# Kernel tuning notes

Hardware: AMD Instinct MI355X
Metric: run time of the kernel (lower is better)

The kernel has to match this reference:

```python
import jax, jax.numpy as jnp
import numpy as np

# init_kwargs constants
K = 5                      # kernel_sz
SIGMA_SPATIAL = 2.0
SIGMA_INTENSITY = 0.1
KVAL = -1.0 / (2.0 * SIGMA_SPATIAL ** 2)        # kernel buffer value (same for all k^2 taps)
SIDIV = 1.0 / (2.0 * SIGMA_INTENSITY ** 2)      # sigma_intensity_div


def _extract_block(x, k):
    """F.unfold equivalent: (B,C,H,W) -> (B,H,W,k*k,C), SAME zero padding, row-major taps."""
    B, C, H, W = x.shape
    p = k // 2
    xp = jnp.pad(x, ((0, 0), (0, 0), (p, p), (p, p)))
    # fixed small loop over k*k taps (not a data-dim loop)
    pats = jnp.stack([xp[:, :, i:i + H, j:j + W] for i in range(k) for j in range(k)], axis=2)  # B,C,k2,H,W
    return jnp.transpose(pats, (0, 3, 4, 2, 1))  # B,H,W,k2,C


def setup_inputs() -> dict:
    key = jax.random.key(0)
    k1, k2 = jax.random.split(key)
    template = jax.random.uniform(k1, (1, 3, 1080, 1920), dtype=jnp.float32)
    vector_curr = jax.random.normal(k2, (1, 2, 1080, 1920), dtype=jnp.float32)
    return {"template": template, "vector_curr": vector_curr}


def reference(template, vector_curr):
    # inputs are float32, so cast() is a no-op
    compare_pix = jnp.transpose(template, (0, 2, 3, 1))[:, :, :, None, :]   # B,H,W,1,C
    compare_kernel = _extract_block(template, K)                            # B,H,W,k2,C
    intensity_diff = jnp.sum((compare_pix - compare_kernel) ** 2, axis=-1)  # B,H,W,k2
    coeff = jnp.clip(1.0 - jnp.abs(KVAL - intensity_diff * SIDIV), 0.0, 1.0)[..., None]  # B,H,W,k2,1
    vector_block = _extract_block(vector_curr, K)                           # B,H,W,k2,Cv
    num = jnp.sum(vector_block * coeff, axis=-2)                            # B,H,W,Cv
    den = jnp.sum(coeff, axis=-2)                                           # B,H,W,1
    out = (num / den).astype(jnp.float16)
    return jnp.transpose(out, (0, 3, 1, 2))                                  # B,Cv,H,W fp16
```

## Files before the change

kernel.cpp:

```cpp
#include <hip/hip_runtime.h>


#define IMG_H 1080
#define IMG_W 1920
#define IMG_HW (IMG_H * IMG_W)
#define TS_X 64
#define TS_Y 16
#define HALO_H 20
#define HALO_W 72
#define NCH 5
#define F4_PER_ROW 18
#define F4_PER_CH  (F4_PER_ROW * HALO_H)

typedef float f4u __attribute__((ext_vector_type(4), aligned(4)));

__global__ __launch_bounds__(256)
void jbf_kernel(const float* __restrict__ tpl,
                const float* __restrict__ vec,
                float* __restrict__ out) {
    constexpr float SIDIV = 50.0f;

    __shared__ __align__(16) float smem[NCH][HALO_H][HALO_W];

    const int tid = threadIdx.x;
    const int x0  = blockIdx.x * TS_X;
    const int y0  = blockIdx.y * TS_Y;

    const bool interior = (blockIdx.x >= 1) & (blockIdx.x <= 28) &
                          (blockIdx.y >= 1) & (blockIdx.y <= 66);

    if (interior) {
        const int i0  = tid;
        const int i1  = tid + 256;
        const bool p1 = (i1 < F4_PER_CH);
        const int i1c = p1 ? i1 : 0;
        const int r0 = i0 / F4_PER_ROW, c0 = i0 - r0 * F4_PER_ROW;
        const int r1 = i1c / F4_PER_ROW, c1 = i1c - r1 * F4_PER_ROW;
        const int off0 = r0 * IMG_W + c0 * 4;
        const int off1 = r1 * IMG_W + c1 * 4;
        const int tl   = (y0 - 2) * IMG_W + (x0 - 2);

        f4u v[2 * NCH];
#pragma unroll
        for (int ch = 0; ch < NCH; ++ch) {
            const float* __restrict__ src =
                (ch < 3) ? (tpl + ch * IMG_HW) : (vec + (ch - 3) * IMG_HW);
            v[2 * ch]     = *(const f4u*)(src + tl + off0);
            v[2 * ch + 1] = *(const f4u*)(src + tl + off1);
        }
#pragma unroll
        for (int ch = 0; ch < NCH; ++ch) {
            float4* d0 = (float4*)&smem[ch][r0][c0 * 4];
            d0->x = v[2 * ch].x; d0->y = v[2 * ch].y;
            d0->z = v[2 * ch].z; d0->w = v[2 * ch].w;
            if (p1) {
                float4* d1 = (float4*)&smem[ch][r1][c1 * 4];
                d1->x = v[2 * ch + 1].x; d1->y = v[2 * ch + 1].y;
                d1->z = v[2 * ch + 1].z; d1->w = v[2 * ch + 1].w;
            }
        }
    } else {
#pragma unroll
        for (int c = 0; c < NCH; ++c) {
            const float* __restrict__ src =
                (c < 3) ? (tpl + c * IMG_HW) : (vec + (c - 3) * IMG_HW);
#pragma unroll
            for (int i = tid; i < HALO_H * HALO_W; i += 256) {
                const int r   = i / HALO_W;
                const int col = i - r * HALO_W;
                const int gy  = y0 + r - 2;
                const int gx  = x0 + col - 2;
                float val = 0.0f;
                if (gy >= 0 && gy < IMG_H && gx >= 0 && gx < IMG_W)
                    val = src[gy * IMG_W + gx];
                smem[c][r][col] = val;
            }
        }
    }
    __syncthreads();

    const int tx = tid & 15;
    const int ty = tid >> 4;
    const int lx = tx * 4;

    float num0[4] = {0.f, 0.f, 0.f, 0.f};
    float num1[4] = {0.f, 0.f, 0.f, 0.f};
    float den [4] = {0.f, 0.f, 0.f, 0.f};
    float c0[4], c1[4], c2[4];

#pragma unroll
    for (int s = 0; s < 5; ++s) {
        constexpr int DYS[5] = {2, 0, 1, 3, 4};
        const int row = ty + DYS[s];
        const float4 a0  = *(const float4*)&smem[0][row][lx];
        const float4 b0  = *(const float4*)&smem[0][row][lx + 4];
        const float4 a1  = *(const float4*)&smem[1][row][lx];
        const float4 b1  = *(const float4*)&smem[1][row][lx + 4];
        const float4 a2  = *(const float4*)&smem[2][row][lx];
        const float4 b2  = *(const float4*)&smem[2][row][lx + 4];
        const float4 av0 = *(const float4*)&smem[3][row][lx];
        const float4 bv0 = *(const float4*)&smem[3][row][lx + 4];
        const float4 av1 = *(const float4*)&smem[4][row][lx];
        const float4 bv1 = *(const float4*)&smem[4][row][lx + 4];

        if (s == 0) {
            c0[0] = a0.z; c0[1] = a0.w; c0[2] = b0.x; c0[3] = b0.y;
            c1[0] = a1.z; c1[1] = a1.w; c1[2] = b1.x; c1[3] = b1.y;
            c2[0] = a2.z; c2[1] = a2.w; c2[2] = b2.x; c2[3] = b2.y;
        }

        const float w0[8]  = {a0.x, a0.y, a0.z, a0.w, b0.x, b0.y, b0.z, b0.w};
        const float w1[8]  = {a1.x, a1.y, a1.z, a1.w, b1.x, b1.y, b1.z, b1.w};
        const float w2[8]  = {a2.x, a2.y, a2.z, a2.w, b2.x, b2.y, b2.z, b2.w};
        const float wv0[8] = {av0.x, av0.y, av0.z, av0.w, bv0.x, bv0.y, bv0.z, bv0.w};
        const float wv1[8] = {av1.x, av1.y, av1.z, av1.w, bv1.x, bv1.y, bv1.z, bv1.w};

#pragma unroll
        for (int dx = 0; dx < 5; ++dx) {
#pragma unroll
            for (int px = 0; px < 4; ++px) {
                const int k = dx + px;
                const float d0 = c0[px] - w0[k];
                const float d1 = c1[px] - w1[k];
                const float d2 = c2[px] - w2[k];
                const float id = fmaf(d0, d0, fmaf(d1, d1, d2 * d2));
                const float coeff = fmaxf(fmaf(id, -SIDIV, 0.875f), 0.0f);
                num0[px] = fmaf(wv0[k], coeff, num0[px]);
                num1[px] = fmaf(wv1[k], coeff, num1[px]);
                den [px] += coeff;
            }
        }
    }

    const int gy = y0 + ty;
    if (gy < IMG_H) {
        const int gx = x0 + lx;
        float4 o0, o1;
        const float r0 = __builtin_amdgcn_rcpf(den[0]);
        const float r1 = __builtin_amdgcn_rcpf(den[1]);
        const float r2 = __builtin_amdgcn_rcpf(den[2]);
        const float r3 = __builtin_amdgcn_rcpf(den[3]);
        o0.x = num0[0] * r0; o0.y = num0[1] * r1; o0.z = num0[2] * r2; o0.w = num0[3] * r3;
        o1.x = num1[0] * r0; o1.y = num1[1] * r1; o1.z = num1[2] * r2; o1.w = num1[3] * r3;
        *(float4*)(out + (size_t)0 * IMG_HW + gy * IMG_W + gx) = o0;
        *(float4*)(out + (size_t)1 * IMG_HW + gy * IMG_W + gx) = o1;
    }
}

extern "C" void kernel_launch(void* const* d_in, const int* in_sizes, int n_in,
                              void* d_out, int out_size, void* d_ws, size_t ws_size,
                              hipStream_t stream) {
    const float* tpl = (const float*)d_in[0];
    const float* vec = (const float*)d_in[1];
    float* out = (float*)d_out;

    dim3 grid(IMG_W / TS_X, (IMG_H + TS_Y - 1) / TS_Y);
    jbf_kernel<<<grid, 256, 0, stream>>>(tpl, vec, out);
}
```

Baseline: 111.4 us.

## Process four row tiles per block with double-buffered LDS prefetch

Each block now walks four vertical tiles, prefetching the next tile's halo into registers before computing the current one and writing it into a second shared-memory buffer afterwards. The aim is to hide global load latency behind compute and amortize per-block setup. In exchange the grid shrinks fourfold, shared memory per block doubles, and register pressure rises, which can reduce occupancy and parallelism across CUs.

```diff
diff --git a/kernel.cpp b/kernel.cpp
--- a/kernel.cpp
+++ b/kernel.cpp
@@ -6,13 +6,57 @@
 #define IMG_HW (IMG_H * IMG_W)
 #define TS_X 64
 #define TS_Y 16
+#define NTILE 4
 #define HALO_H 20
 #define HALO_W 72
 #define NCH 5
 #define F4_PER_ROW 18
-#define F4_PER_CH  (F4_PER_ROW * HALO_H)
+#define F4_PER_CH (F4_PER_ROW * HALO_H)
 
 typedef float f4u __attribute__((ext_vector_type(4), aligned(4)));
+
+#define LOAD_TILE(Y0) do {                                                 \
+    const int tl_ = ((Y0) - 2) * IMG_W + (x0 - 2);                         \
+    _Pragma("unroll")                                                      \
+    for (int ch_ = 0; ch_ < NCH; ++ch_) {                                  \
+        const float* __restrict__ src_ =                                   \
+            (ch_ < 3) ? (tpl + ch_ * IMG_HW) : (vec + (ch_ - 3) * IMG_HW); \
+        v[2 * ch_]     = *(const f4u*)(src_ + tl_ + off0);                 \
+        v[2 * ch_ + 1] = *(const f4u*)(src_ + tl_ + off1);                 \
+    }                                                                      \
+} while (0)
+
+#define WRITE_TILE(BUF) do {                                               \
+    _Pragma("unroll")                                                      \
+    for (int ch_ = 0; ch_ < NCH; ++ch_) {                                  \
+        float4* d0_ = (float4*)&smem[(BUF)][ch_][r0][c0 * 4];              \
+        d0_->x = v[2 * ch_].x; d0_->y = v[2 * ch_].y;                      \
+        d0_->z = v[2 * ch_].z; d0_->w = v[2 * ch_].w;                      \
+        if (p1) {                                                          \
+            float4* d1_ = (float4*)&smem[(BUF)][ch_][r1][c1 * 4];          \
+            d1_->x = v[2 * ch_ + 1].x; d1_->y = v[2 * ch_ + 1].y;          \
+            d1_->z = v[2 * ch_ + 1].z; d1_->w = v[2 * ch_ + 1].w;          \
+        }                                                                  \
+    }                                                                      \
+} while (0)
+
+#define BORDER_STAGE(BUF, Y0) do {                                         \
+    _Pragma("unroll")                                                      \
+    for (int ch_ = 0; ch_ < NCH; ++ch_) {                                  \
+        const float* __restrict__ src_ =                                   \
+            (ch_ < 3) ? (tpl + ch_ * IMG_HW) : (vec + (ch_ - 3) * IMG_HW); \
+        for (int i_ = tid; i_ < HALO_H * HALO_W; i_ += 256) {              \
+            const int r_   = i_ / HALO_W;                                  \
+            const int col_ = i_ - r_ * HALO_W;                             \
+            const int gy_  = (Y0) + r_ - 2;                                \
+            const int gx_  = x0 + col_ - 2;                                \
+            float val_ = 0.0f;                                             \
+            if (gy_ >= 0 && gy_ < IMG_H && gx_ >= 0 && gx_ < IMG_W)        \
+                val_ = src_[gy_ * IMG_W + gx_];                            \
+            smem[(BUF)][ch_][r_][col_] = val_;                             \
+        }                                                                  \
+    }                                                                      \
+} while (0)
 
 __global__ __launch_bounds__(256)
 void jbf_kernel(const float* __restrict__ tpl,
@@ -20,130 +64,125 @@
                 float* __restrict__ out) {
     constexpr float SIDIV = 50.0f;
 
-    __shared__ __align__(16) float smem[NCH][HALO_H][HALO_W];
+    __shared__ __align__(16) float smem[2][NCH][HALO_H][HALO_W];
 
     const int tid = threadIdx.x;
-    const int x0  = blockIdx.x * TS_X;
-    const int y0  = blockIdx.y * TS_Y;
+    const int bx  = blockIdx.x;
+    const int x0  = bx * TS_X;
+    const int yb  = blockIdx.y * (TS_Y * NTILE);
+    const bool xin = (bx >= 1) & (bx <= 28);
 
-    const bool interior = (blockIdx.x >= 1) & (blockIdx.x <= 28) &
-                          (blockIdx.y >= 1) & (blockIdx.y <= 66);
-
-    if (interior) {
-        const int i0  = tid;
-        const int i1  = tid + 256;
-        const bool p1 = (i1 < F4_PER_CH);
-        const int i1c = p1 ? i1 : 0;
-        const int r0 = i0 / F4_PER_ROW, c0 = i0 - r0 * F4_PER_ROW;
-        const int r1 = i1c / F4_PER_ROW, c1 = i1c - r1 * F4_PER_ROW;
-        const int off0 = r0 * IMG_W + c0 * 4;
-        const int off1 = r1 * IMG_W + c1 * 4;
-        const int tl   = (y0 - 2) * IMG_W + (x0 - 2);
-
-        f4u v[2 * NCH];
-#pragma unroll
-        for (int ch = 0; ch < NCH; ++ch) {
-            const float* __restrict__ src =
-                (ch < 3) ? (tpl + ch * IMG_HW) : (vec + (ch - 3) * IMG_HW);
-            v[2 * ch]     = *(const f4u*)(src + tl + off0);
-            v[2 * ch + 1] = *(const f4u*)(src + tl + off1);
-        }
-#pragma unroll
-        for (int ch = 0; ch < NCH; ++ch) {
-            float4* d0 = (float4*)&smem[ch][r0][c0 * 4];
-            d0->x = v[2 * ch].x; d0->y = v[2 * ch].y;
-            d0->z = v[2 * ch].z; d0->w = v[2 * ch].w;
-            if (p1) {
-                float4* d1 = (float4*)&smem[ch][r1][c1 * 4];
-                d1->x = v[2 * ch + 1].x; d1->y = v[2 * ch + 1].y;
-                d1->z = v[2 * ch + 1].z; d1->w = v[2 * ch + 1].w;
-            }
-        }
-    } else {
-#pragma unroll
-        for (int c = 0; c < NCH; ++c) {
-            const float* __restrict__ src =
-                (c < 3) ? (tpl + c * IMG_HW) : (vec + (c - 3) * IMG_HW);
-#pragma unroll
-            for (int i = tid; i < HALO_H * HALO_W; i += 256) {
-                const int r   = i / HALO_W;
-                const int col = i - r * HALO_W;
-                const int gy  = y0 + r - 2;
-                const int gx  = x0 + col - 2;
-                float val = 0.0f;
-                if (gy >= 0 && gy < IMG_H && gx >= 0 && gx < IMG_W)
-                    val = src[gy * IMG_W + gx];
-                smem[c][r][col] = val;
-            }
-        }
-    }
-    __syncthreads();
+    const int i1  = tid + 256;
+    const bool p1 = (i1 < F4_PER_CH);
+    const int i1c = p1 ? i1 : 0;
+    const int r0 = tid / F4_PER_ROW, c0 = tid - r0 * F4_PER_ROW;
+    const int r1 = i1c / F4_PER_ROW, c1 = i1c - r1 * F4_PER_ROW;
+    const int off0 = r0 * IMG_W + c0 * 4;
+    const int off1 = r1 * IMG_W + c1 * 4;
 
     const int tx = tid & 15;
     const int ty = tid >> 4;
     const int lx = tx * 4;
 
-    float num0[4] = {0.f, 0.f, 0.f, 0.f};
-    float num1[4] = {0.f, 0.f, 0.f, 0.f};
-    float den [4] = {0.f, 0.f, 0.f, 0.f};
-    float c0[4], c1[4], c2[4];
+    f4u v[10];
 
-#pragma unroll
-    for (int s = 0; s < 5; ++s) {
-        constexpr int DYS[5] = {2, 0, 1, 3, 4};
-        const int row = ty + DYS[s];
-        const float4 a0  = *(const float4*)&smem[0][row][lx];
-        const float4 b0  = *(const float4*)&smem[0][row][lx + 4];
-        const float4 a1  = *(const float4*)&smem[1][row][lx];
-        const float4 b1  = *(const float4*)&smem[1][row][lx + 4];
-        const float4 a2  = *(const float4*)&smem[2][row][lx];
-        const float4 b2  = *(const float4*)&smem[2][row][lx + 4];
-        const float4 av0 = *(const float4*)&smem[3][row][lx];
-        const float4 bv0 = *(const float4*)&smem[3][row][lx + 4];
-        const float4 av1 = *(const float4*)&smem[4][row][lx];
-        const float4 bv1 = *(const float4*)&smem[4][row][lx + 4];
-
-        if (s == 0) {
-            c0[0] = a0.z; c0[1] = a0.w; c0[2] = b0.x; c0[3] = b0.y;
-            c1[0] = a1.z; c1[1] = a1.w; c1[2] = b1.x; c1[3] = b1.y;
-            c2[0] = a2.z; c2[1] = a2.w; c2[2] = b2.x; c2[3] = b2.y;
-        }
-
-        const float w0[8]  = {a0.x, a0.y, a0.z, a0.w, b0.x, b0.y, b0.z, b0.w};
-        const float w1[8]  = {a1.x, a1.y, a1.z, a1.w, b1.x, b1.y, b1.z, b1.w};
-        const float w2[8]  = {a2.x, a2.y, a2.z, a2.w, b2.x, b2.y, b2.z, b2.w};
-        const float wv0[8] = {av0.x, av0.y, av0.z, av0.w, bv0.x, bv0.y, bv0.z, bv0.w};
-        const float wv1[8] = {av1.x, av1.y, av1.z, av1.w, bv1.x, bv1.y, bv1.z, bv1.w};
-
-#pragma unroll
-        for (int dx = 0; dx < 5; ++dx) {
-#pragma unroll
-            for (int px = 0; px < 4; ++px) {
-                const int k = dx + px;
-                const float d0 = c0[px] - w0[k];
-                const float d1 = c1[px] - w1[k];
-                const float d2 = c2[px] - w2[k];
-                const float id = fmaf(d0, d0, fmaf(d1, d1, d2 * d2));
-                const float coeff = fmaxf(fmaf(id, -SIDIV, 0.875f), 0.0f);
-                num0[px] = fmaf(wv0[k], coeff, num0[px]);
-                num1[px] = fmaf(wv1[k], coeff, num1[px]);
-                den [px] += coeff;
-            }
+    {
+        const int y0 = yb;
+        if (xin & (y0 >= 2) & (y0 + 17 < IMG_H)) {
+            LOAD_TILE(y0);
+            WRITE_TILE(0);
+        } else {
+            BORDER_STAGE(0, y0);
         }
     }
 
-    const int gy = y0 + ty;
-    if (gy < IMG_H) {
-        const int gx = x0 + lx;
-        float4 o0, o1;
-        const float r0 = __builtin_amdgcn_rcpf(den[0]);
-        const float r1 = __builtin_amdgcn_rcpf(den[1]);
-        const float r2 = __builtin_amdgcn_rcpf(den[2]);
-        const float r3 = __builtin_amdgcn_rcpf(den[3]);
-        o0.x = num0[0] * r0; o0.y = num0[1] * r1; o0.z = num0[2] * r2; o0.w = num0[3] * r3;
-        o1.x = num1[0] * r0; o1.y = num1[1] * r1; o1.z = num1[2] * r2; o1.w = num1[3] * r3;
-        *(float4*)(out + (size_t)0 * IMG_HW + gy * IMG_W + gx) = o0;
-        *(float4*)(out + (size_t)1 * IMG_HW + gy * IMG_W + gx) = o1;
+    for (int t = 0; t < NTILE; ++t) {
+        const int cur = t & 1;
+        const int y0  = yb + t * TS_Y;
+        const int yn  = y0 + TS_Y;
+        const bool have_next = (t + 1 < NTILE);
+        const bool int_next  = have_next && xin && (yn + 17 < IMG_H);
+
+        if (int_next) LOAD_TILE(yn);
+        __syncthreads();
+
+        {
+            const float (*S)[HALO_H][HALO_W] =
+                (const float (*)[HALO_H][HALO_W])smem[cur];
+
+            float num0[4] = {0.f, 0.f, 0.f, 0.f};
+            float num1[4] = {0.f, 0.f, 0.f, 0.f};
+            float den [4] = {0.f, 0.f, 0.f, 0.f};
+            float cc0[4], cc1[4], cc2[4];
+
+#pragma unroll
+            for (int s = 0; s < 5; ++s) {
+                constexpr int DYS[5] = {2, 0, 1, 3, 4};
+                const int row = ty + DYS[s];
+                const float4 a0  = *(const float4*)&S[0][row][lx];
+                const float4 b0  = *(const float4*)&S[0][row][lx + 4];
+                const float4 a1  = *(const float4*)&S[1][row][lx];
+                const float4 b1  = *(const float4*)&S[1][row][lx + 4];
+                const float4 a2  = *(const float4*)&S[2][row][lx];
+                const float4 b2  = *(const float4*)&S[2][row][lx + 4];
+                const float4 av0 = *(const float4*)&S[3][row][lx];
+                const float4 bv0 = *(const float4*)&S[3][row][lx + 4];
+                const float4 av1 = *(const float4*)&S[4][row][lx];
+                const float4 bv1 = *(const float4*)&S[4][row][lx + 4];
+
+                if (s == 0) {
+                    cc0[0] = a0.z; cc0[1] = a0.w; cc0[2] = b0.x; cc0[3] = b0.y;
+                    cc1[0] = a1.z; cc1[1] = a1.w; cc1[2] = b1.x; cc1[3] = b1.y;
+                    cc2[0] = a2.z; cc2[1] = a2.w; cc2[2] = b2.x; cc2[3] = b2.y;
+                }
+
+                const float w0[8]  = {a0.x, a0.y, a0.z, a0.w, b0.x, b0.y, b0.z, b0.w};
+                const float w1[8]  = {a1.x, a1.y, a1.z, a1.w, b1.x, b1.y, b1.z, b1.w};
+                const float w2[8]  = {a2.x, a2.y, a2.z, a2.w, b2.x, b2.y, b2.z, b2.w};
+                const float wv0[8] = {av0.x, av0.y, av0.z, av0.w, bv0.x, bv0.y, bv0.z, bv0.w};
+                const float wv1[8] = {av1.x, av1.y, av1.z, av1.w, bv1.x, bv1.y, bv1.z, bv1.w};
+
+#pragma unroll
+                for (int dx = 0; dx < 5; ++dx) {
+#pragma unroll
+                    for (int px = 0; px < 4; ++px) {
+                        const int k = dx + px;
+                        const float d0 = cc0[px] - w0[k];
+                        const float d1 = cc1[px] - w1[k];
+                        const float d2 = cc2[px] - w2[k];
+                        const float id = fmaf(d0, d0, fmaf(d1, d1, d2 * d2));
+                        const float coeff = fmaxf(fmaf(id, -SIDIV, 0.875f), 0.0f);
+                        num0[px] = fmaf(wv0[k], coeff, num0[px]);
+                        num1[px] = fmaf(wv1[k], coeff, num1[px]);
+                        den [px] += coeff;
+                    }
+                }
+            }
+
+            const int gy = y0 + ty;
+            if (gy < IMG_H) {
+                const int gx = x0 + lx;
+                float4 o0, o1;
+                const float q0 = __builtin_amdgcn_rcpf(den[0]);
+                const float q1 = __builtin_amdgcn_rcpf(den[1]);
+                const float q2 = __builtin_amdgcn_rcpf(den[2]);
+                const float q3 = __builtin_amdgcn_rcpf(den[3]);
+                o0.x = num0[0] * q0; o0.y = num0[1] * q1;
+                o0.z = num0[2] * q2; o0.w = num0[3] * q3;
+                o1.x = num1[0] * q0; o1.y = num1[1] * q1;
+                o1.z = num1[2] * q2; o1.w = num1[3] * q3;
+                *(float4*)(out + (size_t)0 * IMG_HW + gy * IMG_W + gx) = o0;
+                *(float4*)(out + (size_t)1 * IMG_HW + gy * IMG_W + gx) = o1;
+            }
+        }
+
+        if (have_next) {
+            if (int_next) {
+                WRITE_TILE(1 - cur);
+            } else {
+                BORDER_STAGE(1 - cur, yn);
+            }
+        }
     }
 }
 
@@ -154,6 +193,6 @@
     const float* vec = (const float*)d_in[1];
     float* out = (float*)d_out;
 
-    dim3 grid(IMG_W / TS_X, (IMG_H + TS_Y - 1) / TS_Y);
+    dim3 grid(IMG_W / TS_X, (IMG_H + TS_Y * NTILE - 1) / (TS_Y * NTILE));
     jbf_kernel<<<grid, 256, 0, stream>>>(tpl, vec, out);
 }
```

New measurement: 136.7 us. 1.23x slower.

## Replace shared-memory halo tiling with direct per-thread global loads

Applied to the files above, without the earlier changes.

Removes the LDS staging of the 5-channel halo tile and the __syncthreads barrier. Each thread now loads its 8-wide row windows straight from global memory for each of the 5 stencil rows, relying on L1/L2 caches for reuse between neighbouring threads. Borders are handled with clamped or masked loads. This cuts LDS traffic and the barrier, but issues more global and cache requests per output, and the row loop is left non-unrolled, which can expose load latency.

```diff
diff --git a/kernel.cpp b/kernel.cpp
--- a/kernel.cpp
+++ b/kernel.cpp
@@ -6,13 +6,82 @@
 #define IMG_HW (IMG_H * IMG_W)
 #define TS_X 64
 #define TS_Y 16
-#define HALO_H 20
-#define HALO_W 72
-#define NCH 5
-#define F4_PER_ROW 18
-#define F4_PER_CH  (F4_PER_ROW * HALO_H)
 
 typedef float f4u __attribute__((ext_vector_type(4), aligned(4)));
+
+#define UNPACK8(dst, A, B) \
+    dst[0]=(A).x; dst[1]=(A).y; dst[2]=(A).z; dst[3]=(A).w; \
+    dst[4]=(B).x; dst[5]=(B).y; dst[6]=(B).z; dst[7]=(B).w;
+
+#define LOAD_FAST(ROW) do {                                                   \
+    const float* p_ = tpl + (ROW) * IMG_W + (gx - 2);                         \
+    const float* q_ = vec + (ROW) * IMG_W + (gx - 2);                         \
+    const f4u a0_  = *(const f4u*)(p_);                                       \
+    const f4u b0_  = *(const f4u*)(p_ + 4);                                   \
+    const f4u a1_  = *(const f4u*)(p_ + IMG_HW);                              \
+    const f4u b1_  = *(const f4u*)(p_ + IMG_HW + 4);                          \
+    const f4u a2_  = *(const f4u*)(p_ + 2 * IMG_HW);                          \
+    const f4u b2_  = *(const f4u*)(p_ + 2 * IMG_HW + 4);                      \
+    const f4u av0_ = *(const f4u*)(q_);                                       \
+    const f4u bv0_ = *(const f4u*)(q_ + 4);                                   \
+    const f4u av1_ = *(const f4u*)(q_ + IMG_HW);                              \
+    const f4u bv1_ = *(const f4u*)(q_ + IMG_HW + 4);                          \
+    UNPACK8(w0,  a0_,  b0_)  UNPACK8(w1,  a1_,  b1_)                          \
+    UNPACK8(w2,  a2_,  b2_)  UNPACK8(wv0, av0_, bv0_)                         \
+    UNPACK8(wv1, av1_, bv1_)                                                  \
+} while (0)
+
+#define LOAD_CLAMPY(ROW) do {                                                 \
+    const int   rc_ = (ROW) < 0 ? 0 : ((ROW) > IMG_H - 1 ? IMG_H - 1 : (ROW));\
+    const float m_  = ((ROW) >= 0 && (ROW) < IMG_H) ? 1.0f : 0.0f;            \
+    LOAD_FAST(rc_);                                                           \
+    _Pragma("unroll")                                                         \
+    for (int k_ = 0; k_ < 8; ++k_) {                                          \
+        w0[k_] *= m_; w1[k_] *= m_; w2[k_] *= m_;                             \
+        wv0[k_] *= m_; wv1[k_] *= m_;                                         \
+    }                                                                         \
+} while (0)
+
+#define LOAD_SLOW(ROW) do {                                                   \
+    const bool rv_ = ((ROW) >= 0) & ((ROW) < IMG_H);                          \
+    const int  rb_ = (rv_ ? (ROW) : 0) * IMG_W;                               \
+    _Pragma("unroll")                                                         \
+    for (int k_ = 0; k_ < 8; ++k_) {                                          \
+        const int   col_ = gx - 2 + k_;                                       \
+        const bool  v_   = rv_ & (col_ >= 0) & (col_ < IMG_W);                \
+        const int   ic_  = rb_ + (v_ ? col_ : 0);                             \
+        const float m_   = v_ ? 1.0f : 0.0f;                                  \
+        w0[k_]  = m_ * tpl[ic_];                                              \
+        w1[k_]  = m_ * tpl[ic_ + IMG_HW];                                     \
+        w2[k_]  = m_ * tpl[ic_ + 2 * IMG_HW];                                 \
+        wv0[k_] = m_ * vec[ic_];                                              \
+        wv1[k_] = m_ * vec[ic_ + IMG_HW];                                     \
+    }                                                                         \
+} while (0)
+
+#define LOAD_ROW(ROW) do {                                                    \
+    if (xin & yin)  LOAD_FAST(ROW);                                           \
+    else if (xin)   LOAD_CLAMPY(ROW);                                         \
+    else            LOAD_SLOW(ROW);                                           \
+} while (0)
+
+#define TAPS do {                                                             \
+    _Pragma("unroll")                                                         \
+    for (int dx = 0; dx < 5; ++dx) {                                          \
+        _Pragma("unroll")                                                     \
+        for (int px = 0; px < 4; ++px) {                                      \
+            const int   k  = dx + px;                                         \
+            const float d0 = c0[px] - w0[k];                                  \
+            const float d1 = c1[px] - w1[k];                                  \
+            const float d2 = c2[px] - w2[k];                                  \
+            const float id = fmaf(d0, d0, fmaf(d1, d1, d2 * d2));             \
+            const float coeff = fmaxf(fmaf(id, -SIDIV, 0.875f), 0.0f);        \
+            num0[px] = fmaf(wv0[k], coeff, num0[px]);                         \
+            num1[px] = fmaf(wv1[k], coeff, num1[px]);                         \
+            den [px] += coeff;                                                \
+        }                                                                     \
+    }                                                                         \
+} while (0)
 
 __global__ __launch_bounds__(256)
 void jbf_kernel(const float* __restrict__ tpl,
@@ -20,121 +89,35 @@
                 float* __restrict__ out) {
     constexpr float SIDIV = 50.0f;
 
-    __shared__ __align__(16) float smem[NCH][HALO_H][HALO_W];
+    const int tid = threadIdx.x;
+    const int tx  = tid & 15;
+    const int ty  = tid >> 4;
+    const int gx  = blockIdx.x * TS_X + tx * 4;
+    const int gy  = blockIdx.y * TS_Y + ty;
 
-    const int tid = threadIdx.x;
-    const int x0  = blockIdx.x * TS_X;
-    const int y0  = blockIdx.y * TS_Y;
-
-    const bool interior = (blockIdx.x >= 1) & (blockIdx.x <= 28) &
-                          (blockIdx.y >= 1) & (blockIdx.y <= 66);
-
-    if (interior) {
-        const int i0  = tid;
-        const int i1  = tid + 256;
-        const bool p1 = (i1 < F4_PER_CH);
-        const int i1c = p1 ? i1 : 0;
-        const int r0 = i0 / F4_PER_ROW, c0 = i0 - r0 * F4_PER_ROW;
-        const int r1 = i1c / F4_PER_ROW, c1 = i1c - r1 * F4_PER_ROW;
-        const int off0 = r0 * IMG_W + c0 * 4;
-        const int off1 = r1 * IMG_W + c1 * 4;
-        const int tl   = (y0 - 2) * IMG_W + (x0 - 2);
-
-        f4u v[2 * NCH];
-#pragma unroll
-        for (int ch = 0; ch < NCH; ++ch) {
-            const float* __restrict__ src =
-                (ch < 3) ? (tpl + ch * IMG_HW) : (vec + (ch - 3) * IMG_HW);
-            v[2 * ch]     = *(const f4u*)(src + tl + off0);
-            v[2 * ch + 1] = *(const f4u*)(src + tl + off1);
-        }
-#pragma unroll
-        for (int ch = 0; ch < NCH; ++ch) {
-            float4* d0 = (float4*)&smem[ch][r0][c0 * 4];
-            d0->x = v[2 * ch].x; d0->y = v[2 * ch].y;
-            d0->z = v[2 * ch].z; d0->w = v[2 * ch].w;
-            if (p1) {
-                float4* d1 = (float4*)&smem[ch][r1][c1 * 4];
-                d1->x = v[2 * ch + 1].x; d1->y = v[2 * ch + 1].y;
-                d1->z = v[2 * ch + 1].z; d1->w = v[2 * ch + 1].w;
-            }
-        }
-    } else {
-#pragma unroll
-        for (int c = 0; c < NCH; ++c) {
-            const float* __restrict__ src =
-                (c < 3) ? (tpl + c * IMG_HW) : (vec + (c - 3) * IMG_HW);
-#pragma unroll
-            for (int i = tid; i < HALO_H * HALO_W; i += 256) {
-                const int r   = i / HALO_W;
-                const int col = i - r * HALO_W;
-                const int gy  = y0 + r - 2;
-                const int gx  = x0 + col - 2;
-                float val = 0.0f;
-                if (gy >= 0 && gy < IMG_H && gx >= 0 && gx < IMG_W)
-                    val = src[gy * IMG_W + gx];
-                smem[c][r][col] = val;
-            }
-        }
-    }
-    __syncthreads();
-
-    const int tx = tid & 15;
-    const int ty = tid >> 4;
-    const int lx = tx * 4;
+    const bool xin = (blockIdx.x >= 1) & (blockIdx.x <= 28);
+    const bool yin = (blockIdx.y >= 1) & (blockIdx.y <= 66);
 
     float num0[4] = {0.f, 0.f, 0.f, 0.f};
     float num1[4] = {0.f, 0.f, 0.f, 0.f};
     float den [4] = {0.f, 0.f, 0.f, 0.f};
     float c0[4], c1[4], c2[4];
+    float w0[8], w1[8], w2[8], wv0[8], wv1[8];
 
-#pragma unroll
-    for (int s = 0; s < 5; ++s) {
-        constexpr int DYS[5] = {2, 0, 1, 3, 4};
-        const int row = ty + DYS[s];
-        const float4 a0  = *(const float4*)&smem[0][row][lx];
-        const float4 b0  = *(const float4*)&smem[0][row][lx + 4];
-        const float4 a1  = *(const float4*)&smem[1][row][lx];
-        const float4 b1  = *(const float4*)&smem[1][row][lx + 4];
-        const float4 a2  = *(const float4*)&smem[2][row][lx];
-        const float4 b2  = *(const float4*)&smem[2][row][lx + 4];
-        const float4 av0 = *(const float4*)&smem[3][row][lx];
-        const float4 bv0 = *(const float4*)&smem[3][row][lx + 4];
-        const float4 av1 = *(const float4*)&smem[4][row][lx];
-        const float4 bv1 = *(const float4*)&smem[4][row][lx + 4];
+    LOAD_ROW(gy);
+    c0[0] = w0[2]; c0[1] = w0[3]; c0[2] = w0[4]; c0[3] = w0[5];
+    c1[0] = w1[2]; c1[1] = w1[3]; c1[2] = w1[4]; c1[3] = w1[5];
+    c2[0] = w2[2]; c2[1] = w2[3]; c2[2] = w2[4]; c2[3] = w2[5];
+    TAPS;
 
-        if (s == 0) {
-            c0[0] = a0.z; c0[1] = a0.w; c0[2] = b0.x; c0[3] = b0.y;
-            c1[0] = a1.z; c1[1] = a1.w; c1[2] = b1.x; c1[3] = b1.y;
-            c2[0] = a2.z; c2[1] = a2.w; c2[2] = b2.x; c2[3] = b2.y;
-        }
-
-        const float w0[8]  = {a0.x, a0.y, a0.z, a0.w, b0.x, b0.y, b0.z, b0.w};
-        const float w1[8]  = {a1.x, a1.y, a1.z, a1.w, b1.x, b1.y, b1.z, b1.w};
-        const float w2[8]  = {a2.x, a2.y, a2.z, a2.w, b2.x, b2.y, b2.z, b2.w};
-        const float wv0[8] = {av0.x, av0.y, av0.z, av0.w, bv0.x, bv0.y, bv0.z, bv0.w};
-        const float wv1[8] = {av1.x, av1.y, av1.z, av1.w, bv1.x, bv1.y, bv1.z, bv1.w};
-
-#pragma unroll
-        for (int dx = 0; dx < 5; ++dx) {
-#pragma unroll
-            for (int px = 0; px < 4; ++px) {
-                const int k = dx + px;
-                const float d0 = c0[px] - w0[k];
-                const float d1 = c1[px] - w1[k];
-                const float d2 = c2[px] - w2[k];
-                const float id = fmaf(d0, d0, fmaf(d1, d1, d2 * d2));
-                const float coeff = fmaxf(fmaf(id, -SIDIV, 0.875f), 0.0f);
-                num0[px] = fmaf(wv0[k], coeff, num0[px]);
-                num1[px] = fmaf(wv1[k], coeff, num1[px]);
-                den [px] += coeff;
-            }
-        }
+#pragma unroll 1
+    for (int j = 0; j < 4; ++j) {
+        const int dy = j + (j >> 1);
+        LOAD_ROW(gy + dy - 2);
+        TAPS;
     }
 
-    const int gy = y0 + ty;
     if (gy < IMG_H) {
-        const int gx = x0 + lx;
         float4 o0, o1;
         const float r0 = __builtin_amdgcn_rcpf(den[0]);
         const float r1 = __builtin_amdgcn_rcpf(den[1]);
```

Result: slower. 117.9 us (+5.8%).
